# Kernel tuning notes

Measured on AMD Instinct MI355X. Metric: run time of the kernel, lower is better.

## Reference

```python
import jax, jax.numpy as jnp
import numpy as np

N, D, O = 8000, 9, 1  # mulElements hard-codes 8000 rows; fc: 9 -> 1


def setup_inputs() -> dict:
    key = jax.random.key(0)
    ks = jax.random.split(key, 5)
    # scale x small so the (buggy) cumulative product over 8000 rows stays finite/nonzero
    x = jax.random.normal(ks[0], (N, D), dtype=jnp.float32) * 1e-3
    a1 = jnp.array([1.0], dtype=jnp.float32)
    c1 = jnp.array([0.0], dtype=jnp.float32)
    a2 = jnp.array([1.1], dtype=jnp.float32)
    c2 = jnp.array([5e-4], dtype=jnp.float32)
    w_fc1 = jax.random.normal(ks[1], (O, D), dtype=jnp.float32) / np.sqrt(D)
    b_fc1 = jax.random.normal(ks[2], (O,), dtype=jnp.float32) * 0.01
    w_fc2 = jax.random.normal(ks[3], (O, D), dtype=jnp.float32) / np.sqrt(D)
    b_fc2 = jax.random.normal(ks[4], (O,), dtype=jnp.float32) * 0.01
    return {"x": x, "a1": a1, "c1": c1, "a2": a2, "c2": c2,
            "w_fc1": w_fc1, "b_fc1": b_fc1, "w_fc2": w_fc2, "b_fc2": b_fc2}


def reference(x, a1, c1, a2, c2, w_fc1, b_fc1, w_fc2, b_fc2):
    # Gaussian memberships, [N, D]
    miu1 = jnp.exp(-(((x - c1) / a1) ** 2))
    miu2 = jnp.exp(-(((x - c2) / a2) ** 2))
    # mulElements: w_temp is NOT reset per row in the original code, so
    # w[i] = prod over rows 0..i of the row-product -> cumprod of row products.
    w1 = jnp.cumprod(jnp.prod(miu1, axis=1))  # [N]
    w2 = jnp.cumprod(jnp.prod(miu2, axis=1))  # [N]
    s = w1 + w2
    w1_bar = w1 / s  # [N]
    w2_bar = w2 / s  # [N]
    f1 = x @ w_fc1.T + b_fc1  # [N, 1]
    f2 = x @ w_fc2.T + b_fc2  # [N, 1]
    # torch broadcasting: [N] * [N,1] -> [N,N]
    out = f1 * w1_bar[None, :] + f2 * w2_bar[None, :]  # [N, N]
    return out
```

## Files before the change

### kernel.cpp

```cpp
#include <hip/hip_runtime.h>

#define NROWS 8000
#define DDIM 9
#define NCOL4 (NROWS / 4)
#define ROWS_PER_BLK 50
#define NCHUNK 125

typedef float f32x4 __attribute__((ext_vector_type(4)));

__global__ __launch_bounds__(256)
void anfis_rows(const float* __restrict__ x,
                const float* __restrict__ a1p, const float* __restrict__ c1p,
                const float* __restrict__ a2p, const float* __restrict__ c2p,
                const float* __restrict__ w_fc1, const float* __restrict__ b_fc1,
                const float* __restrict__ w_fc2, const float* __restrict__ b_fc2,
                float* __restrict__ cs1o, float* __restrict__ cs2o,
                float2* __restrict__ f12o,
                float* __restrict__ t1o, float* __restrict__ t2o) {
    const int wid  = (blockIdx.x * 256 + threadIdx.x) >> 6;
    const int lane = threadIdx.x & 63;
    if (wid >= NCHUNK) return;
    const int r = wid * 64 + lane;

    const float inv_a1 = 1.0f / a1p[0];
    const float c1 = c1p[0];
    const float inv_a2 = 1.0f / a2p[0];
    const float c2 = c2p[0];

    float s1 = 0.f, s2 = 0.f, d1 = 0.f, d2 = 0.f;
#pragma unroll
    for (int j = 0; j < DDIM; ++j) {
        float xv = x[r * DDIM + j];
        float u1 = (xv - c1) * inv_a1;
        float u2 = (xv - c2) * inv_a2;
        s1 += u1 * u1;
        s2 += u2 * u2;
        d1 += xv * w_fc1[j];
        d2 += xv * w_fc2[j];
    }
    f12o[r] = make_float2(d1 + b_fc1[0], d2 + b_fc2[0]);

#pragma unroll
    for (int d = 1; d < 64; d <<= 1) {
        float n1 = __shfl_up(s1, d, 64);
        float n2 = __shfl_up(s2, d, 64);
        if (lane >= d) { s1 += n1; s2 += n2; }
    }
    cs1o[r] = s1;
    cs2o[r] = s2;
    if (lane == 63) { t1o[wid] = s1; t2o[wid] = s2; }
}

__global__ __launch_bounds__(256)
void anfis_out(const float2* __restrict__ f12,
               const float* __restrict__ cs1, const float* __restrict__ cs2,
               const float* __restrict__ t1, const float* __restrict__ t2,
               float* __restrict__ out) {
    __shared__ float sp1[128];
    __shared__ float sp2[128];
    __shared__ float2 sf[ROWS_PER_BLK];
    const int tid = threadIdx.x;
    const int i0 = blockIdx.y * ROWS_PER_BLK;

    if (tid < ROWS_PER_BLK) sf[tid] = f12[i0 + tid];

    if (tid < 64) {
        const int l = tid;
        float e10 = 0.f, e11 = 0.f, e20 = 0.f, e21 = 0.f;
        if (2 * l < NCHUNK)     { e10 = t1[2 * l];     e20 = t2[2 * l]; }
        if (2 * l + 1 < NCHUNK) { e11 = t1[2 * l + 1]; e21 = t2[2 * l + 1]; }
        const float p1 = e10 + e11, p2 = e20 + e21;
        float s1 = p1, s2 = p2;
#pragma unroll
        for (int d = 1; d < 64; d <<= 1) {
            float n1 = __shfl_up(s1, d, 64);
            float n2 = __shfl_up(s2, d, 64);
            if (l >= d) { s1 += n1; s2 += n2; }
        }
        const float ex1 = s1 - p1, ex2 = s2 - p2;
        sp1[2 * l]     = ex1;        sp2[2 * l]     = ex2;
        sp1[2 * l + 1] = ex1 + e10;  sp2[2 * l + 1] = ex2 + e20;
    }
    __syncthreads();

    const int j4 = blockIdx.x * 256 + tid;
    if (j4 >= NCOL4) return;
    const int c = j4 >> 4;

    f32x4 u, v;
    {
        f32x4 a = ((const f32x4*)cs1)[j4] + sp1[c];
        f32x4 b = ((const f32x4*)cs2)[j4] + sp2[c];
#pragma unroll
        for (int q = 0; q < 4; ++q) {
            float e = expf(a[q] - b[q]);
            float inv = 1.0f / (1.0f + e);
            u[q] = inv;
            v[q] = e * inv;
        }
    }

    f32x4* orow = (f32x4*)out + (size_t)i0 * NCOL4 + j4;
#pragma unroll 5
    for (int k = 0; k < ROWS_PER_BLK; ++k) {
        const float2 ab = sf[k];
        *orow = ab.x * u + ab.y * v;
        orow += NCOL4;
    }
}

extern "C" void kernel_launch(void* const* d_in, const int* in_sizes, int n_in,
                              void* d_out, int out_size, void* d_ws, size_t ws_size,
                              hipStream_t stream) {
    const float* x     = (const float*)d_in[0];
    const float* a1    = (const float*)d_in[1];
    const float* c1    = (const float*)d_in[2];
    const float* a2    = (const float*)d_in[3];
    const float* c2    = (const float*)d_in[4];
    const float* w_fc1 = (const float*)d_in[5];
    const float* b_fc1 = (const float*)d_in[6];
    const float* w_fc2 = (const float*)d_in[7];
    const float* b_fc2 = (const float*)d_in[8];
    float* out = (float*)d_out;

    float* ws   = (float*)d_ws;
    float* cs1  = ws;
    float* cs2  = ws + 8000;
    float2* f12 = (float2*)(ws + 16000);
    float* t1   = ws + 32000;
    float* t2   = ws + 32125;

    anfis_rows<<<(NCHUNK * 64 + 255) / 256, 256, 0, stream>>>(
        x, a1, c1, a2, c2, w_fc1, b_fc1, w_fc2, b_fc2, cs1, cs2, f12, t1, t2);
    anfis_out<<<dim3((NCOL4 + 255) / 256, NROWS / ROWS_PER_BLK), 256, 0, stream>>>(
        f12, cs1, cs2, t1, t2, out);
}
```

Baseline: 263.9 us.

## Split column weights into separate kernel and write full output rows per block

Column normalisation weights are now computed once by a new kernel and stored to workspace, rather than recomputed by every row-block. The output kernel holds a whole row's worth of weights in registers and writes 5 complete contiguous rows per block. It also uses the identity v = 1 - u to cut the per-element work to one FMA. This adds a third kernel launch and a workspace round-trip for the weights, and changes the block shape of the store-bound output kernel.

```diff
diff --git a/kernel.cpp b/kernel.cpp
--- a/kernel.cpp
+++ b/kernel.cpp
@@ -3,8 +3,10 @@
 #define NROWS 8000
 #define DDIM 9
 #define NCOL4 (NROWS / 4)
-#define ROWS_PER_BLK 50
 #define NCHUNK 125
+#define ROWS_PER_BLK 5
+#define NPASS 7
+#define TAIL 208
 
 typedef float f32x4 __attribute__((ext_vector_type(4)));
 
@@ -52,17 +54,12 @@
 }
 
 __global__ __launch_bounds__(256)
-void anfis_out(const float2* __restrict__ f12,
-               const float* __restrict__ cs1, const float* __restrict__ cs2,
-               const float* __restrict__ t1, const float* __restrict__ t2,
-               float* __restrict__ out) {
+void anfis_cols(const float* __restrict__ cs1, const float* __restrict__ cs2,
+                const float* __restrict__ t1, const float* __restrict__ t2,
+                f32x4* __restrict__ u4) {
     __shared__ float sp1[128];
     __shared__ float sp2[128];
-    __shared__ float2 sf[ROWS_PER_BLK];
     const int tid = threadIdx.x;
-    const int i0 = blockIdx.y * ROWS_PER_BLK;
-
-    if (tid < ROWS_PER_BLK) sf[tid] = f12[i0 + tid];
 
     if (tid < 64) {
         const int l = tid;
@@ -87,25 +84,38 @@
     if (j4 >= NCOL4) return;
     const int c = j4 >> 4;
 
-    f32x4 u, v;
-    {
-        f32x4 a = ((const f32x4*)cs1)[j4] + sp1[c];
-        f32x4 b = ((const f32x4*)cs2)[j4] + sp2[c];
+    f32x4 a = ((const f32x4*)cs1)[j4] + sp1[c];
+    f32x4 b = ((const f32x4*)cs2)[j4] + sp2[c];
+    f32x4 u;
 #pragma unroll
-        for (int q = 0; q < 4; ++q) {
-            float e = expf(a[q] - b[q]);
-            float inv = 1.0f / (1.0f + e);
-            u[q] = inv;
-            v[q] = e * inv;
-        }
+    for (int q = 0; q < 4; ++q) {
+        float e = expf(a[q] - b[q]);
+        u[q] = 1.0f / (1.0f + e);
     }
+    u4[j4] = u;
+}
 
-    f32x4* orow = (f32x4*)out + (size_t)i0 * NCOL4 + j4;
-#pragma unroll 5
-    for (int k = 0; k < ROWS_PER_BLK; ++k) {
-        const float2 ab = sf[k];
-        *orow = ab.x * u + ab.y * v;
-        orow += NCOL4;
+__global__ __launch_bounds__(256)
+void anfis_out(const float2* __restrict__ f12, const f32x4* __restrict__ u4,
+               float* __restrict__ out) {
+    const int tid = threadIdx.x;
+    const int i0 = blockIdx.x * ROWS_PER_BLK;
+
+    f32x4 ur[NPASS + 1];
+#pragma unroll
+    for (int p = 0; p < NPASS; ++p) ur[p] = u4[tid + p * 256];
+    if (tid < TAIL) ur[NPASS] = u4[tid + NPASS * 256];
+
+#pragma unroll
+    for (int r = 0; r < ROWS_PER_BLK; ++r) {
+        const float2 ab = f12[i0 + r];
+        const float d = ab.x - ab.y;
+        f32x4* row = (f32x4*)out + (size_t)(i0 + r) * NCOL4;
+#pragma unroll
+        for (int p = 0; p < NPASS; ++p)
+            row[tid + p * 256] = d * ur[p] + ab.y;
+        if (tid < TAIL)
+            row[tid + NPASS * 256] = d * ur[NPASS] + ab.y;
     }
 }
 
@@ -129,9 +139,10 @@
     float2* f12 = (float2*)(ws + 16000);
     float* t1   = ws + 32000;
     float* t2   = ws + 32125;
+    f32x4* u4   = (f32x4*)(ws + 32256);
 
     anfis_rows<<<(NCHUNK * 64 + 255) / 256, 256, 0, stream>>>(
         x, a1, c1, a2, c2, w_fc1, b_fc1, w_fc2, b_fc2, cs1, cs2, f12, t1, t2);
-    anfis_out<<<dim3((NCOL4 + 255) / 256, NROWS / ROWS_PER_BLK), 256, 0, stream>>>(
-        f12, cs1, cs2, t1, t2, out);
+    anfis_cols<<<(NCOL4 + 255) / 256, 256, 0, stream>>>(cs1, cs2, t1, t2, u4);
+    anfis_out<<<NROWS / ROWS_PER_BLK, 256, 0, stream>>>(f12, u4, out);
 }
```

Result: no change. 265.2 us (+0.5%).
